# Kernel optimization log

Hardware: AMD Instinct MI355X
Metric: run time of the kernel (lower is better)

The kernel has to match this reference:

```python
import jax, jax.numpy as jnp
import numpy as np

# 2^22-point radix-2 DIT FFT; NOTE the original code applies tf.abs at EVERY
# recursion level (not just the top), so each butterfly stage is followed by a
# magnitude + recomplexification. We reproduce that exact (non-standard) math.
N = 1 << 22
STAGES = 22


def _bitrev_perm(n, bits):
    # vectorized bit-reversal permutation (the order induced by the even/odd
    # decimation inputs[0::2] / inputs[1::2] recursion)
    x = np.arange(n)
    r = np.zeros(n, dtype=np.int64)
    for b in range(bits):
        r = (r << 1) | ((x >> b) & 1)
    return r


_PERM = jnp.asarray(_bitrev_perm(N, STAGES))


def setup_inputs() -> dict:
    key = jax.random.key(0)
    x = jax.random.normal(key, (N,), dtype=jnp.float32)
    return {"x": x}


def reference(x):
    # base case of the recursion: length-1 leaves are the bit-reversed inputs
    y = x[_PERM].astype(jnp.complex64)
    for s in range(1, STAGES + 1):  # fixed log2(N) stages, not a data loop
        m = 1 << s                  # sub-FFT size at this stage
        yb = y.reshape(N // m, m)   # [num_blocks, m]
        e = yb[:, : m // 2]         # 'even' sub-results
        o = yb[:, m // 2:]          # 'odd'  sub-results
        # twiddles W(m, k) = exp(-2*pi*i*k/m)
        tw = jnp.exp(
            jnp.complex64(-2j * np.pi) * jnp.arange(m // 2, dtype=jnp.float32) / m
        ).astype(jnp.complex64)
        t = tw[None, :] * o
        # butterfly then tf.abs (applied at every level in the original)
        mag = jnp.abs(jnp.concatenate([e + t, e - t], axis=1)).reshape(N)
        y = mag.astype(jnp.complex64) if s < STAGES else mag
    return y  # float32 magnitudes, shape [N]
```

## Files before the change

kernel.cpp:

```cpp
#include <hip/hip_runtime.h>
#include <math.h>


#define NBITS 22

__device__ __forceinline__ void bf(float& e, float& o, float c, float s) {
    float co = c * o, im = s * o;
    float rp = e + co, rm = e - co;
    float im2 = im * im;
    e = __builtin_amdgcn_sqrtf(fmaf(rp, rp, im2));
    o = __builtin_amdgcn_sqrtf(fmaf(rm, rm, im2));
}

__device__ __forceinline__ void cs(float r, float& c, float& s) {
    c = __builtin_amdgcn_cosf(r);
    s = __builtin_amdgcn_sinf(r);
}

__device__ __forceinline__ void radix8(float v[8], float b0, float b1, float b2) {
    float c, s;
    cs(b0, c, s);
    bf(v[0], v[1], c, s); bf(v[2], v[3], c, s);
    bf(v[4], v[5], c, s); bf(v[6], v[7], c, s);
    cs(b1, c, s);
    bf(v[0], v[2], c, s); bf(v[4], v[6], c, s);
    cs(b1 + 0.25f, c, s);
    bf(v[1], v[3], c, s); bf(v[5], v[7], c, s);
    cs(b2, c, s);           bf(v[0], v[4], c, s);
    cs(b2 + 0.125f, c, s);  bf(v[1], v[5], c, s);
    cs(b2 + 0.25f, c, s);   bf(v[2], v[6], c, s);
    cs(b2 + 0.375f, c, s);  bf(v[3], v[7], c, s);
}

#define PAD(i) ((i) + ((i) >> 3))

__global__ __launch_bounds__(1024, 8) void fft_low(const float* __restrict__ x,
                                                   float* __restrict__ y) {
    __shared__ float lds[9216];
    const unsigned t = threadIdx.x;
    const unsigned base = blockIdx.x * 8192;
    float v[8];

#pragma unroll
    for (int j = 0; j < 8; ++j) {
        unsigned p = base + t * 8 + j;
        v[j] = x[__brev(p) >> (32 - NBITS)];
    }
    radix8(v, 0.f, 0.f, 0.f);
#pragma unroll
    for (int j = 0; j < 8; ++j) lds[PAD(t * 8 + j)] = v[j];
    __syncthreads();

    {
        const unsigned lo = t & 7, hi = t >> 3;
        const unsigned i0 = hi * 64 + lo;
#pragma unroll
        for (int j = 0; j < 8; ++j) v[j] = lds[PAD(i0 + j * 8)];
        const float f = (float)lo;
        radix8(v, f * (1.f/16), f * (1.f/32), f * (1.f/64));
#pragma unroll
        for (int j = 0; j < 8; ++j) lds[PAD(i0 + j * 8)] = v[j];
    }
    __syncthreads();

    {
        const unsigned lo = t & 63, hi = t >> 6;
        const unsigned i0 = hi * 512 + lo;
#pragma unroll
        for (int j = 0; j < 8; ++j) v[j] = lds[PAD(i0 + j * 64)];
        const float f = (float)lo;
        radix8(v, f * (1.f/128), f * (1.f/256), f * (1.f/512));
#pragma unroll
        for (int j = 0; j < 8; ++j) lds[PAD(i0 + j * 64)] = v[j];
    }
    __syncthreads();

    {
        const unsigned lo = t & 511, hi = t >> 9;
        const unsigned i0 = hi * 4096 + lo;
#pragma unroll
        for (int j = 0; j < 8; ++j) v[j] = lds[PAD(i0 + j * 512)];
        const float f = (float)lo;
        radix8(v, f * (1.f/1024), f * (1.f/2048), f * (1.f/4096));
#pragma unroll
        for (int j = 0; j < 8; ++j) lds[PAD(i0 + j * 512)] = v[j];
    }
    __syncthreads();

#pragma unroll
    for (int it = 0; it < 4; ++it) {
        const unsigned i = it * 1024 + t;
        float e = lds[PAD(i)];
        float o = lds[PAD(i + 4096)];
        float c, s;
        cs((float)i * (1.f/8192), c, s);
        bf(e, o, c, s);
        y[base + i] = e;
        y[base + i + 4096] = o;
    }
}

__global__ __launch_bounds__(1024, 8) void fft_high(float* __restrict__ y) {
    __shared__ float lds[512 * 17 + 16];
    const unsigned tt = threadIdx.x;
    const unsigned li = tt & 15, u = tt >> 4;
    const unsigned low = blockIdx.x * 16 + li;
    float v[8];

#pragma unroll
    for (int j = 0; j < 8; ++j) v[j] = y[low + 8192u * (u * 8 + j)];
    {
        const float K = (float)low;
        radix8(v, K * (1.f/16384), K * (1.f/32768), K * (1.f/65536));
    }
#pragma unroll
    for (int j = 0; j < 8; ++j) lds[(u * 8 + j) * 17 + li] = v[j];
    __syncthreads();

    {
        const unsigned lo8 = u & 7, hi = u >> 3;
        const unsigned t0 = hi * 64 + lo8;
#pragma unroll
        for (int j = 0; j < 8; ++j) v[j] = lds[(t0 + j * 8) * 17 + li];
        const float K = (float)low + 8192.f * (float)lo8;
        radix8(v, K * (1.f/131072), K * (1.f/262144), K * (1.f/524288));
#pragma unroll
        for (int j = 0; j < 8; ++j) lds[(t0 + j * 8) * 17 + li] = v[j];
    }
    __syncthreads();

    {
#pragma unroll
        for (int j = 0; j < 8; ++j) v[j] = lds[(u + j * 64) * 17 + li];
        const float K = (float)low + 8192.f * (float)u;
        radix8(v, K * (1.f/1048576), K * (1.f/2097152), K * (1.f/4194304));
#pragma unroll
        for (int j = 0; j < 8; ++j) y[low + 8192u * (u + j * 64)] = v[j];
    }
}

extern "C" void kernel_launch(void* const* d_in, const int* in_sizes, int n_in,
                              void* d_out, int out_size, void* d_ws, size_t ws_size,
                              hipStream_t stream) {
    const float* x = (const float*)d_in[0];
    float* out = (float*)d_out;

    fft_low<<<dim3(512), dim3(1024), 0, stream>>>(x, out);
    fft_high<<<dim3(512), dim3(1024), 0, stream>>>(out);
}
```

Measured before the change: 104.3 us.

## Split bit-reversal gather into a tiled LDS transpose kernel

Adds a separate permutation kernel that performs the bit-reversal gather through a padded 64x64 shared-memory tile, so global reads and writes are coalesced, and also does the first radix-8 pass there. The low-stage kernel then reads contiguous float4 data instead of scattered bit-reversed addresses. Launch-bound occupancy hints change from 8 to 4 on the two existing kernels. The cost is an extra kernel launch and an extra full read and write pass over the 16 MB array.

New measurement: 101.2 us. 3.0% less time.

```diff
diff --git a/kernel.cpp b/kernel.cpp
--- a/kernel.cpp
+++ b/kernel.cpp
@@ -34,19 +34,47 @@
 
 #define PAD(i) ((i) + ((i) >> 3))
 
-__global__ __launch_bounds__(1024, 8) void fft_low(const float* __restrict__ x,
-                                                   float* __restrict__ y) {
+__global__ __launch_bounds__(256) void fft_perm(const float* __restrict__ x,
+                                                float* __restrict__ y) {
+    __shared__ float lds[64 * 65];
+    const unsigned tid = threadIdx.x;
+    const unsigned tx = tid & 63, g = tid >> 6;
+    const unsigned C0 = (blockIdx.x & 31) * 64;
+    const unsigned B0 = (blockIdx.x >> 5) * 64;
+
+#pragma unroll
+    for (int k = 0; k < 16; ++k) {
+        unsigned r = g * 16 + k;
+        unsigned a = __brev(C0 + r) >> (32 - 11);
+        lds[r * 65 + tx] = x[a * 2048u + B0 + tx];
+    }
+    __syncthreads();
+
+    float v[8];
+#pragma unroll
+    for (int q = 0; q < 2; ++q) {
+        unsigned task = tid + 256u * q;
+        unsigned c = task >> 3, grp = task & 7;
+#pragma unroll
+        for (int j = 0; j < 8; ++j) v[j] = lds[(grp * 8 + j) * 65 + c];
+        radix8(v, 0.f, 0.f, 0.f);
+        unsigned pr = __brev(B0 + c) >> (32 - 11);
+        float* dst = y + pr * 2048u + C0 + grp * 8;
+        *(float4*)(dst)     = make_float4(v[0], v[1], v[2], v[3]);
+        *(float4*)(dst + 4) = make_float4(v[4], v[5], v[6], v[7]);
+    }
+}
+
+__global__ __launch_bounds__(1024, 4) void fft_low(float* __restrict__ y) {
     __shared__ float lds[9216];
     const unsigned t = threadIdx.x;
     const unsigned base = blockIdx.x * 8192;
     float v[8];
 
-#pragma unroll
-    for (int j = 0; j < 8; ++j) {
-        unsigned p = base + t * 8 + j;
-        v[j] = x[__brev(p) >> (32 - NBITS)];
-    }
-    radix8(v, 0.f, 0.f, 0.f);
+    const float4* src = (const float4*)(y + base + t * 8);
+    float4 u0 = src[0], u1 = src[1];
+    v[0] = u0.x; v[1] = u0.y; v[2] = u0.z; v[3] = u0.w;
+    v[4] = u1.x; v[5] = u1.y; v[6] = u1.z; v[7] = u1.w;
 #pragma unroll
     for (int j = 0; j < 8; ++j) lds[PAD(t * 8 + j)] = v[j];
     __syncthreads();
@@ -100,7 +128,7 @@
     }
 }
 
-__global__ __launch_bounds__(1024, 8) void fft_high(float* __restrict__ y) {
+__global__ __launch_bounds__(1024, 4) void fft_high(float* __restrict__ y) {
     __shared__ float lds[512 * 17 + 16];
     const unsigned tt = threadIdx.x;
     const unsigned li = tt & 15, u = tt >> 4;
@@ -145,6 +173,7 @@
     const float* x = (const float*)d_in[0];
     float* out = (float*)d_out;
 
-    fft_low<<<dim3(512), dim3(1024), 0, stream>>>(x, out);
+    fft_perm<<<dim3(1024), dim3(256), 0, stream>>>(x, out);
+    fft_low<<<dim3(512), dim3(1024), 0, stream>>>(out);
     fft_high<<<dim3(512), dim3(1024), 0, stream>>>(out);
 }
```
